# Kernel optimization log

Hardware: AMD Instinct MI355X
Metric: run time of the kernel (lower is better)

The kernel has to match this reference:

```python
import jax, jax.numpy as jnp
import numpy as np

B, N, D, H, C = 32, 512, 256, 256, 2
EPS_NEIGH = 0.3
VSN = 1e-12
SMOOTH_R, DEGREE_R, SPARSITY_R = 0.2, 0.0, 0.1


def setup_inputs() -> dict:
    key = jax.random.key(0)
    ks = jax.random.split(key, 12)
    s = 0.02
    return {
        "context": jax.random.normal(ks[0], (B, N, D), jnp.float32),
        "attention_mask": jnp.ones((B, N, 1), jnp.int32),
        "W_gcn": jax.random.normal(ks[1], (D, H), jnp.float32) * s,
        "b_gcn": jnp.zeros((H,), jnp.float32),
        "W_att1": jax.random.normal(ks[2], (H, H), jnp.float32) * s,
        "b_att1": jnp.zeros((H,), jnp.float32),
        "ln_g": jnp.ones((H,), jnp.float32),
        "ln_b": jnp.zeros((H,), jnp.float32),
        "W_att2": jax.random.normal(ks[3], (H, 1), jnp.float32) * s,
        "b_att2": jnp.zeros((1,), jnp.float32),
        "W_out": jax.random.normal(ks[4], (H, C), jnp.float32) * s,
        "b_out": jnp.zeros((C,), jnp.float32),
    }


def reference(context, attention_mask, W_gcn, b_gcn, W_att1, b_att1,
              ln_g, ln_b, W_att2, b_att2, W_out, b_out):
    # --- GraphLearner (cosine metric + epsilon neighbourhood) ---
    cn = context / jnp.maximum(
        jnp.linalg.norm(context, axis=-1, keepdims=True), VSN)
    att = jnp.einsum('bnd,bmd->bnm', cn, cn)              # [B,N,N]
    mask = jax.lax.stop_gradient((att > EPS_NEIGH).astype(att.dtype))
    adj = att * mask                                      # markoff_value = 0

    # --- GCN diffusion (row-normalized adjacency) ---
    row = adj.sum(-1, keepdims=True)                      # [B,N,1]
    adj_norm = adj / (row + VSN)
    h = jax.nn.relu(
        jnp.einsum('bnm,bmd->bnd', adj_norm, context) @ W_gcn + b_gcn)

    # --- AttentionNetPooling: Linear -> LayerNorm -> GELU -> Linear(1) ---
    a = h @ W_att1 + b_att1
    mu = a.mean(-1, keepdims=True)
    var = a.var(-1, keepdims=True)
    a = (a - mu) / jnp.sqrt(var + 1e-5) * ln_g + ln_b
    w = jax.nn.gelu(a, approximate=False) @ W_att2 + b_att2   # [B,N,1]
    w = jnp.where(attention_mask == 0, -jnp.inf, w)
    w = jax.nn.softmax(w, axis=1)
    pooled = jnp.sum(w * h, axis=1)                       # [B,H]
    logits = pooled @ W_out + b_out                       # [B,C]

    # --- add_batch_graph_loss (L = diag(rowsum) - adj, topk = N) ---
    Lx = row * context - jnp.einsum('bnm,bmd->bnd', adj, context)
    smooth = SMOOTH_R * jnp.mean(
        jnp.sum(context * Lx, axis=(-1, -2)) / (N * N))
    deg = -DEGREE_R * jnp.mean(
        jnp.sum(jnp.log(row[..., 0] + VSN), axis=-1) / N)
    sparsity = SPARSITY_R * jnp.sum(adj ** 2) / (N * N) / B
    graph_loss = smooth + deg + sparsity
    return logits, graph_loss
```

## Files before the change

### kernel.cpp

```cpp
#include <hip/hip_runtime.h>
#include <math.h>

#define NS 512
#define ND 256
#define LIST_CAP 32768u

typedef short short8 __attribute__((ext_vector_type(8)));
typedef float f32x16 __attribute__((ext_vector_type(16)));

__device__ __forceinline__ unsigned short bf16_rne(float x) {
  unsigned u = __float_as_uint(x);
  unsigned r = u + 0x7fffu + ((u >> 16) & 1u);
  return (unsigned short)(r >> 16);
}
__device__ __forceinline__ float bf16_tof(unsigned short h) {
  return __uint_as_float(((unsigned)h) << 16);
}
__device__ __forceinline__ void bsplit(float x, unsigned short& h, unsigned short& l) {
  h = bf16_rne(x);
  l = bf16_rne(x - bf16_tof(h));
}
__device__ __forceinline__ float wave_sum(float v) {
  v += __shfl_xor(v, 1);  v += __shfl_xor(v, 2);  v += __shfl_xor(v, 4);
  v += __shfl_xor(v, 8);  v += __shfl_xor(v, 16); v += __shfl_xor(v, 32);
  return v;
}

__device__ __forceinline__ void gload_lds16(const void* g, void* l) {
  __builtin_amdgcn_global_load_lds(
      (const __attribute__((address_space(1))) unsigned int*)g,
      (__attribute__((address_space(3))) unsigned int*)l, 16, 0, 0);
}

__device__ __forceinline__ void stage4(const unsigned short* __restrict__ hiA,
                                       const unsigned short* __restrict__ loA, int grA,
                                       const unsigned short* __restrict__ hiB,
                                       const unsigned short* __restrict__ loB, int grB,
                                       int k0, char* lds, int wid, int lane)
{
  #pragma unroll
  for (int q = 0; q < 2; ++q) {
    const int c = (q * 4 + wid) * 64 + lane;
    const int row = c >> 3;
    const int soff = ((c & 7) * 16) ^ ((row & 7) << 4);
    const int dest = (q * 4 + wid) * 1024;
    const size_t ga = (size_t)(grA + row) * ND + k0 + (soff >> 1);
    const size_t gb = (size_t)(grB + row) * ND + k0 + (soff >> 1);
    gload_lds16(hiA + ga, lds + dest);
    gload_lds16(loA + ga, lds + 8192 + dest);
    gload_lds16(hiB + gb, lds + 16384 + dest);
    gload_lds16(loB + gb, lds + 24576 + dest);
  }
}

#define SWZB(row, off) (((row) << 7) + (((off) ^ (((row) & 7) << 4))))

#define STEP_MFMA(lds, arow, brow) do { \
  _Pragma("unroll") \
  for (int ks = 0; ks < 4; ++ks) { \
    const int off = ks * 32 + hl * 16; \
    short8 ah = *(const short8*)((lds) + SWZB((arow), off)); \
    short8 al = *(const short8*)((lds) + 8192 + SWZB((arow), off)); \
    short8 bh = *(const short8*)((lds) + 16384 + SWZB((brow), off)); \
    short8 bl = *(const short8*)((lds) + 24576 + SWZB((brow), off)); \
    acc = __builtin_amdgcn_mfma_f32_32x32x16_bf16(ah, bh, acc, 0, 0, 0); \
    acc = __builtin_amdgcn_mfma_f32_32x32x16_bf16(ah, bl, acc, 0, 0, 0); \
    acc = __builtin_amdgcn_mfma_f32_32x32x16_bf16(al, bh, acc, 0, 0, 0); \
  } \
} while (0)

__device__ __forceinline__ float pdot_raw(const float* __restrict__ ctx,
                                          const float* __restrict__ Wg,
                                          int row, int t) {
  const float* cr = ctx + (size_t)row * ND;
  float a = 0.f;
  #pragma unroll 16
  for (int k = 0; k < ND; ++k) a = fmaf(cr[k], Wg[(size_t)k * ND + t], a);
  return a;
}

__global__ __launch_bounds__(256)
void k_prep(const float* __restrict__ ctx, const float* __restrict__ Wg,
            const float* __restrict__ Wa,
            float* __restrict__ nrm, float* __restrict__ nsq,
            unsigned short* __restrict__ cnhi, unsigned short* __restrict__ cnlo,
            unsigned short* __restrict__ wgthi, unsigned short* __restrict__ wgtlo,
            unsigned short* __restrict__ wathi, unsigned short* __restrict__ watlo,
            unsigned* __restrict__ cnt)
{
  if (blockIdx.x >= 4096) {
    int wb = blockIdx.x - 4096;
    int j = wb & 255, selA = wb >> 8;
    int k = threadIdx.x;
    if (wb == 0 && k == 0) *cnt = 0u;
    const float* W = selA ? Wa : Wg;
    unsigned short h, l;
    bsplit(W[k * ND + j], h, l);
    if (selA) { wathi[j * ND + k] = h; watlo[j * ND + k] = l; }
    else      { wgthi[j * ND + k] = h; wgtlo[j * ND + k] = l; }
    return;
  }
  int w = threadIdx.x >> 6, lane = threadIdx.x & 63;
  int g = blockIdx.x * 4 + w;
  float4 v = ((const float4*)ctx)[(size_t)g * 64 + lane];
  float ss = v.x*v.x + v.y*v.y + v.z*v.z + v.w*v.w;
  ss = wave_sum(ss);
  float n = sqrtf(ss);
  float rn = 1.f / fmaxf(n, 1e-12f);
  if (lane == 0) { nrm[g] = n; nsq[g] = ss; }
  ushort4 hi, lo;
  bsplit(v.x * rn, hi.x, lo.x);
  bsplit(v.y * rn, hi.y, lo.y);
  bsplit(v.z * rn, hi.z, lo.z);
  bsplit(v.w * rn, hi.w, lo.w);
  ((ushort4*)cnhi)[(size_t)g * 64 + lane] = hi;
  ((ushort4*)cnlo)[(size_t)g * 64 + lane] = lo;
}

__global__ __launch_bounds__(256, 4)
void k_gram2(const unsigned short* __restrict__ cnhi, const unsigned short* __restrict__ cnlo,
             const float* __restrict__ nrm,
             float* __restrict__ rowp, float* __restrict__ diag,
             float* __restrict__ pA2, float* __restrict__ pA3,
             unsigned* __restrict__ cnt, unsigned* __restrict__ keys,
             float* __restrict__ vals)
{
  __shared__ __align__(16) char lds[32768];
  __shared__ float s_row[2][64];
  __shared__ float s_col[2][64];
  __shared__ float sred[8];
  const int bx0 = blockIdx.x;
  const int bx = (bx0 & 7) * 144 + (bx0 >> 3);
  const int b = bx / 36;
  int rem = bx % 36, ti = 0;
  #pragma unroll
  for (int q = 0; q < 7; ++q) { if (rem >= 8 - ti) { rem -= 8 - ti; ++ti; } }
  const int tj = ti + rem;
  const bool diagT = (ti == tj);
  const int i0 = ti * 64, j0 = tj * 64;
  const int bB = b * NS;
  const int rbA = bB + i0, rbB = bB + j0;

  const int tid = threadIdx.x;
  const int lane = tid & 63, wid = tid >> 6;
  const int l31 = lane & 31, hl = lane >> 5;
  const int wr = wid >> 1, wc = wid & 1;
  const int arow = wr * 32 + l31;
  const int brow = wc * 32 + l31;

  f32x16 acc = {};
  #pragma unroll
  for (int t = 0; t < 4; ++t) {
    stage4(cnhi, cnlo, rbA, cnhi, cnlo, rbB, t * 64, lds, wid, lane);
    __syncthreads();
    STEP_MFMA(lds, arow, brow);
    __syncthreads();
  }

  const float nc = nrm[rbB + wc * 32 + l31];
  const int gcol = wc * 32 + l31;
  float a2 = 0.f, a3 = 0.f, colsum = 0.f;

  #pragma unroll
  for (int r = 0; r < 16; ++r) {
    const int rofs = (r & 3) + 8 * (r >> 2) + 4 * hl;
    const int grow = wr * 32 + rofs;
    const float nr = nrm[rbA + grow];
    float v = acc[r];
    float adj = (v > 0.3f) ? v : 0.f;
    float q2 = adj * adj;
    a3 += q2;
    a2 += q2 * nr * nc;
    colsum += adj;
    if (diagT) {
      if (grow == gcol) {
        diag[bB + i0 + grow] = adj;
      } else if (adj > 0.f) {
        unsigned idx = atomicAdd(cnt, 1u);
        if (idx < LIST_CAP) {
          keys[idx] = (unsigned)((bB + i0 + grow) * NS + (j0 + gcol));
          vals[idx] = adj;
        }
      }
    } else if (adj > 0.f) {
      unsigned idx = atomicAdd(cnt, 2u);
      if (idx < LIST_CAP) {
        keys[idx] = (unsigned)((bB + i0 + grow) * NS + (j0 + gcol));
        vals[idx] = adj;
      }
      if (idx + 1u < LIST_CAP) {
        keys[idx + 1u] = (unsigned)((bB + j0 + gcol) * NS + (i0 + grow));
        vals[idx + 1u] = adj;
      }
    }
    float rs = adj;
    rs += __shfl_xor(rs, 1); rs += __shfl_xor(rs, 2); rs += __shfl_xor(rs, 4);
    rs += __shfl_xor(rs, 8); rs += __shfl_xor(rs, 16);
    if (l31 == 0) s_row[wc][grow] = rs;
  }
  colsum += __shfl_xor(colsum, 32);
  if (!diagT && hl == 0) s_col[wr][gcol] = colsum;
  a2 = wave_sum(a2);
  a3 = wave_sum(a3);
  if (lane == 0) { sred[wid] = a2; sred[4 + wid] = a3; }
  __syncthreads();
  if (tid < 64) {
    rowp[tj * 16384 + rbA + tid] = s_row[0][tid] + s_row[1][tid];
    if (!diagT)
      rowp[ti * 16384 + rbB + tid] = s_col[0][tid] + s_col[1][tid];
  }
  if (tid == 0) {
    float f = diagT ? 1.f : 2.f;
    pA2[bx] = f * (sred[0] + sred[1] + sred[2] + sred[3]);
    pA3[bx] = f * (sred[4] + sred[5] + sred[6] + sred[7]);
  }
}

__global__ __launch_bounds__(256, 4)
void k_pgemm(const unsigned short* __restrict__ cnhi, const unsigned short* __restrict__ cnlo,
             const unsigned short* __restrict__ wgthi, const unsigned short* __restrict__ wgtlo,
             const float* __restrict__ rowp, const float* __restrict__ nrm,
             const float* __restrict__ nsq, const float* __restrict__ diag,
             const float* __restrict__ b_gcn,
             unsigned short* __restrict__ Hhi, unsigned short* __restrict__ Hlo,
             float* __restrict__ pA1)
{
  __shared__ __align__(16) char lds[32768];
  __shared__ float lss[64];
  const int i0 = blockIdx.x * 64;
  const int c0 = blockIdx.y * 64;
  const int tid = threadIdx.x;
  const int lane = tid & 63, wid = tid >> 6;
  const int l31 = lane & 31, hl = lane >> 5;
  const int wr = wid >> 1, wc = wid & 1;
  const int arow = wr * 32 + l31;
  const int brow = wc * 32 + l31;

  if (tid < 64) {
    int g = i0 + tid;
    float r = 0.f;
    #pragma unroll
    for (int s2 = 0; s2 < 8; ++s2) r += rowp[s2 * 16384 + g];
    float rr = 1.f / (r + 1e-12f);
    lss[tid] = nrm[g] * diag[g] * rr;
    float v = r * nsq[g];
    v = wave_sum(v);
    if (tid == 0 && blockIdx.y == 0) pA1[blockIdx.x] = v;
  }

  f32x16 acc = {};
  #pragma unroll
  for (int t = 0; t < 4; ++t) {
    stage4(cnhi, cnlo, i0, wgthi, wgtlo, c0, t * 64, lds, wid, lane);
    __syncthreads();
    STEP_MFMA(lds, arow, brow);
    __syncthreads();
  }

  const int gcol = c0 + wc * 32 + l31;
  const float bv = b_gcn[gcol];
  #pragma unroll
  for (int r = 0; r < 16; ++r) {
    const int rofs = (r & 3) + 8 * (r >> 2) + 4 * hl;
    const int lrow = wr * 32 + rofs;
    const size_t grow = (size_t)(i0 + lrow);
    float v = fmaxf(lss[lrow] * acc[r] + bv, 0.f);
    unsigned short h, l;
    bsplit(v, h, l);
    Hhi[grow * ND + gcol] = h;
    Hlo[grow * ND + gcol] = l;
  }
}

__global__ __launch_bounds__(256)
void k_fix(const float* __restrict__ ctx, const float* __restrict__ Wg,
           const float* __restrict__ rowp, const float* __restrict__ diag,
           const float* __restrict__ b_gcn,
           const unsigned* __restrict__ cnt, const unsigned* __restrict__ keys,
           const float* __restrict__ vals,
           unsigned short* __restrict__ Hhi, unsigned short* __restrict__ Hlo)
{
  unsigned c = *cnt; if (c > LIST_CAP) c = LIST_CAP;
  unsigned e = blockIdx.x;
  if (e >= c) return;
  int bn = (int)(keys[e] >> 9);
  for (unsigned e2 = 0; e2 < e; ++e2)
    if ((int)(keys[e2] >> 9) == bn) return;
  int t = threadIdx.x;
  float r = 0.f;
  #pragma unroll
  for (int s2 = 0; s2 < 8; ++s2) r += rowp[s2 * 16384 + bn];
  float rr = 1.f / (r + 1e-12f);
  float pre = diag[bn] * rr * pdot_raw(ctx, Wg, bn, t) + b_gcn[t];
  for (unsigned e2 = e; e2 < c; ++e2) {
    unsigned k2 = keys[e2];
    if ((int)(k2 >> 9) != bn) continue;
    int bm = (bn & ~511) | (int)(k2 & 511u);
    pre += vals[e2] * rr * pdot_raw(ctx, Wg, bm, t);
  }
  float hv = fmaxf(pre, 0.f);
  unsigned short hh, ll;
  bsplit(hv, hh, ll);
  Hhi[(size_t)bn * ND + t] = hh;
  Hlo[(size_t)bn * ND + t] = ll;
}

__global__ __launch_bounds__(256, 4)
void k_mm1(const unsigned short* __restrict__ Ahi, const unsigned short* __restrict__ Alo,
           const unsigned short* __restrict__ Bthi, const unsigned short* __restrict__ Btlo,
           const float* __restrict__ bias, float* __restrict__ outf)
{
  __shared__ __align__(16) char lds[32768];
  const int i0 = blockIdx.x * 64;
  const int c0 = blockIdx.y * 64;
  const int tid = threadIdx.x;
  const int lane = tid & 63, wid = tid >> 6;
  const int l31 = lane & 31, hl = lane >> 5;
  const int wr = wid >> 1, wc = wid & 1;
  const int arow = wr * 32 + l31;
  const int brow = wc * 32 + l31;

  f32x16 acc = {};
  #pragma unroll
  for (int t = 0; t < 4; ++t) {
    stage4(Ahi, Alo, i0, Bthi, Btlo, c0, t * 64, lds, wid, lane);
    __syncthreads();
    STEP_MFMA(lds, arow, brow);
    __syncthreads();
  }

  const int gcol = c0 + wc * 32 + l31;
  const float bv = bias[gcol];
  #pragma unroll
  for (int r = 0; r < 16; ++r) {
    const int rofs = (r & 3) + 8 * (r >> 2) + 4 * hl;
    const size_t grow = (size_t)(i0 + wr * 32 + rofs);
    outf[grow * ND + gcol] = acc[r] + bv;
  }
}

__global__ __launch_bounds__(256)
void k_ln(const float* __restrict__ a, const float* __restrict__ g,
          const float* __restrict__ bt, const float* __restrict__ W2,
          const float* __restrict__ b2, float* __restrict__ wl)
{
  int w = threadIdx.x >> 6, lane = threadIdx.x & 63;
  int row = blockIdx.x * 4 + w;
  float4 x = ((const float4*)a)[(size_t)row * 64 + lane];
  float s = x.x + x.y + x.z + x.w;
  float ss = fmaf(x.x, x.x, fmaf(x.y, x.y, fmaf(x.z, x.z, x.w * x.w)));
  s = wave_sum(s); ss = wave_sum(ss);
  float mu = s * (1.f / 256.f);
  float var = ss * (1.f / 256.f) - mu * mu;
  float rstd = rsqrtf(fmaxf(var, 0.f) + 1e-5f);
  float4 gg = ((const float4*)g)[lane];
  float4 bb = ((const float4*)bt)[lane];
  float4 wv = ((const float4*)W2)[lane];
  const float inv_sqrt2 = 0.70710678118654752f;
  float d = 0.f;
  float y = (x.x - mu) * rstd * gg.x + bb.x;
  d = fmaf(0.5f * y * (1.f + erff(y * inv_sqrt2)), wv.x, d);
  y = (x.y - mu) * rstd * gg.y + bb.y;
  d = fmaf(0.5f * y * (1.f + erff(y * inv_sqrt2)), wv.y, d);
  y = (x.z - mu) * rstd * gg.z + bb.z;
  d = fmaf(0.5f * y * (1.f + erff(y * inv_sqrt2)), wv.z, d);
  y = (x.w - mu) * rstd * gg.w + bb.w;
  d = fmaf(0.5f * y * (1.f + erff(y * inv_sqrt2)), wv.w, d);
  d = wave_sum(d);
  if (lane == 0) wl[row] = d + b2[0];
}

__global__ __launch_bounds__(512)
void k_poolfin(const float* __restrict__ wl, const int* __restrict__ amask,
               const unsigned short* __restrict__ Hhi, const unsigned short* __restrict__ Hlo,
               const float* __restrict__ W_out, const float* __restrict__ b_out,
               const float* __restrict__ pA1, const float* __restrict__ pA2,
               const float* __restrict__ pA3, float* __restrict__ out)
{
  __shared__ float red[512];
  __shared__ float sw[512];
  __shared__ float pp[512];
  const int t = threadIdx.x;
  if (blockIdx.x < 32) {
    const int b = blockIdx.x;
    float l = (amask[b * NS + t] == 0) ? -INFINITY : wl[b * NS + t];
    red[t] = l;
    __syncthreads();
    for (int s = 256; s; s >>= 1) { if (t < s) red[t] = fmaxf(red[t], red[t + s]); __syncthreads(); }
    float mx = red[0];
    __syncthreads();
    float e = expf(l - mx);
    red[t] = e;
    __syncthreads();
    for (int s = 256; s; s >>= 1) { if (t < s) red[t] += red[t + s]; __syncthreads(); }
    float inv = 1.f / red[0];
    sw[t] = e * inv;
    __syncthreads();
    const int col = t & 255, half = t >> 8;
    const size_t hb = ((size_t)b * NS + (size_t)half * 256) * ND + col;
    float acc = 0.f;
    #pragma unroll 8
    for (int n = 0; n < 256; ++n) {
      float hv = bf16_tof(Hhi[hb + (size_t)n * ND]) + bf16_tof(Hlo[hb + (size_t)n * ND]);
      acc = fmaf(sw[half * 256 + n], hv, acc);
    }
    pp[t] = acc;
    __syncthreads();
    if (t < 256) {
      float pool = pp[t] + pp[256 + t];
      red[t] = pool * W_out[t * 2 + 0];
      red[256 + t] = pool * W_out[t * 2 + 1];
    }
    __syncthreads();
    for (int s = 128; s; s >>= 1) {
      if (t < s) { red[t] += red[t + s]; red[256 + t] += red[256 + t + s]; }
      __syncthreads();
    }
    if (t == 0) {
      out[b * 2 + 0] = red[0] + b_out[0];
      out[b * 2 + 1] = red[256] + b_out[1];
    }
  } else {
    float r1 = (t < 256) ? pA1[t] : 0.f;
    float r2 = pA2[t] + pA2[512 + t] + ((t < 128) ? pA2[1024 + t] : 0.f);
    float r3 = pA3[t] + pA3[512 + t] + ((t < 128) ? pA3[1024 + t] : 0.f);
    red[t] = r1;
    __syncthreads();
    for (int s = 256; s; s >>= 1) { if (t < s) red[t] += red[t + s]; __syncthreads(); }
    r1 = red[0];
    __syncthreads();
    red[t] = r2;
    __syncthreads();
    for (int s = 256; s; s >>= 1) { if (t < s) red[t] += red[t + s]; __syncthreads(); }
    r2 = red[0];
    __syncthreads();
    red[t] = r3;
    __syncthreads();
    for (int s = 256; s; s >>= 1) { if (t < s) red[t] += red[t + s]; __syncthreads(); }
    if (t == 0) {
      float smooth = 0.2f * (r1 - r2) * (1.f / (32.f * 512.f * 512.f));
      float spars  = 0.1f * red[0] * (1.f / (512.f * 512.f)) * (1.f / 32.f);
      out[64] = smooth + spars;
    }
  }
}

extern "C" void kernel_launch(void* const* d_in, const int* in_sizes, int n_in,
                              void* d_out, int out_size, void* d_ws, size_t ws_size,
                              hipStream_t stream)
{
  (void)in_sizes; (void)n_in; (void)out_size; (void)ws_size;
  const float* ctx    = (const float*)d_in[0];
  const int*   amask  = (const int*)d_in[1];
  const float* W_gcn  = (const float*)d_in[2];
  const float* b_gcn  = (const float*)d_in[3];
  const float* W_att1 = (const float*)d_in[4];
  const float* b_att1 = (const float*)d_in[5];
  const float* ln_g   = (const float*)d_in[6];
  const float* ln_b   = (const float*)d_in[7];
  const float* W_att2 = (const float*)d_in[8];
  const float* b_att2 = (const float*)d_in[9];
  const float* W_out  = (const float*)d_in[10];
  const float* b_out  = (const float*)d_in[11];
  float* out = (float*)d_out;

  float* ws = (float*)d_ws;
  unsigned short* cnhi = (unsigned short*)ws;
  unsigned short* cnlo = (unsigned short*)(ws + 2097152);
  unsigned short* Hhi  = (unsigned short*)(ws + 4194304);
  unsigned short* Hlo  = (unsigned short*)(ws + 4194304 + 2097152);
  float* abuf = ws + 8388608;
  float* sp   = ws + 12582912;
  float* nrm  = sp;            sp += 16384;
  float* nsq  = sp;            sp += 16384;
  float* rowp = sp;            sp += 131072;
  float* diag = sp;            sp += 16384;
  float* wl   = sp;            sp += 16384;
  float* pA1  = sp;            sp += 4096;
  float* pA2  = sp;            sp += 1280;
  float* pA3  = sp;            sp += 1280;
  unsigned* cnt  = (unsigned*)sp;  sp += 64;
  unsigned* keys = (unsigned*)sp;  sp += 32768;
  float* vals = sp;            sp += 32768;
  unsigned short* wgthi = (unsigned short*)sp; sp += 32768;
  unsigned short* wgtlo = (unsigned short*)sp; sp += 32768;
  unsigned short* wathi = (unsigned short*)sp; sp += 32768;
  unsigned short* watlo = (unsigned short*)sp; sp += 32768;

  k_prep<<<4608, 256, 0, stream>>>(ctx, W_gcn, W_att1, nrm, nsq, cnhi, cnlo,
                                   wgthi, wgtlo, wathi, watlo, cnt);
  k_gram2<<<1152, 256, 0, stream>>>(cnhi, cnlo, nrm, rowp, diag, pA2, pA3,
                                    cnt, keys, vals);
  k_pgemm<<<dim3(256, 4), 256, 0, stream>>>(cnhi, cnlo, wgthi, wgtlo, rowp,
                                            nrm, nsq, diag, b_gcn, Hhi, Hlo, pA1);
  k_fix<<<256, 256, 0, stream>>>(ctx, W_gcn, rowp, diag, b_gcn,
                                 cnt, keys, vals, Hhi, Hlo);
  k_mm1<<<dim3(256, 4), 256, 0, stream>>>(Hhi, Hlo, wathi, watlo, b_att1, abuf);
  k_ln<<<4096, 256, 0, stream>>>(abuf, ln_g, ln_b, W_att2, b_att2, wl);
  k_poolfin<<<33, 512, 0, stream>>>(wl, amask, Hhi, Hlo, W_out, b_out,
                                    pA1, pA2, pA3, out);
}
```

Before: 97.87 us.

## Split attention pooling across 512 blocks with a separate final reduction kernel

The single 33-block pooling/finalize kernel becomes two kernels. The first uses 512 blocks, each recomputing the per-batch softmax and summing a 32-row slice of H into a partial buffer that reuses the cn workspace. The second reduces the 16 partials per batch, applies W_out, and folds in the graph-loss partial sums. The aim is to fill the GPU during the H read instead of leaving most CUs idle, at the cost of an extra launch and redundant softmax work in every block.

```diff
diff --git a/kernel.cpp b/kernel.cpp
--- a/kernel.cpp
+++ b/kernel.cpp
@@ -370,73 +370,81 @@
   if (lane == 0) wl[row] = d + b2[0];
 }
 
-__global__ __launch_bounds__(512)
-void k_poolfin(const float* __restrict__ wl, const int* __restrict__ amask,
-               const unsigned short* __restrict__ Hhi, const unsigned short* __restrict__ Hlo,
-               const float* __restrict__ W_out, const float* __restrict__ b_out,
-               const float* __restrict__ pA1, const float* __restrict__ pA2,
-               const float* __restrict__ pA3, float* __restrict__ out)
+__global__ __launch_bounds__(256)
+void k_pool2(const float* __restrict__ wl, const int* __restrict__ amask,
+             const unsigned short* __restrict__ hhi, const unsigned short* __restrict__ hlo,
+             float* __restrict__ part)
+{
+  __shared__ float sw[512];
+  __shared__ float red[256];
+  int b = blockIdx.x >> 4, p = blockIdx.x & 15, t = threadIdx.x;
+  float l0 = (amask[b * NS + t]       == 0) ? -INFINITY : wl[b * NS + t];
+  float l1 = (amask[b * NS + 256 + t] == 0) ? -INFINITY : wl[b * NS + 256 + t];
+  red[t] = fmaxf(l0, l1);
+  __syncthreads();
+  for (int s = 128; s; s >>= 1) { if (t < s) red[t] = fmaxf(red[t], red[t + s]); __syncthreads(); }
+  float mx = red[0];
+  __syncthreads();
+  float e0 = expf(l0 - mx), e1 = expf(l1 - mx);
+  red[t] = e0 + e1;
+  __syncthreads();
+  for (int s = 128; s; s >>= 1) { if (t < s) red[t] += red[t + s]; __syncthreads(); }
+  float inv = 1.f / red[0];
+  sw[t] = e0 * inv; sw[256 + t] = e1 * inv;
+  __syncthreads();
+  const size_t base = (size_t)b * NS * ND + (size_t)p * 32 * ND + t;
+  float acc = 0.f;
+  #pragma unroll 8
+  for (int n = 0; n < 32; ++n) {
+    float hv = bf16_tof(hhi[base + (size_t)n * ND]) + bf16_tof(hlo[base + (size_t)n * ND]);
+    acc = fmaf(sw[p * 32 + n], hv, acc);
+  }
+  part[(size_t)blockIdx.x * ND + t] = acc;
+}
+
+__global__ __launch_bounds__(256)
+void k_final(const float* __restrict__ part, const float* __restrict__ W_out,
+             const float* __restrict__ b_out, const float* __restrict__ pA1,
+             const float* __restrict__ pA2, const float* __restrict__ pA3,
+             float* __restrict__ out)
 {
   __shared__ float red[512];
-  __shared__ float sw[512];
-  __shared__ float pp[512];
-  const int t = threadIdx.x;
+  int t = threadIdx.x;
   if (blockIdx.x < 32) {
-    const int b = blockIdx.x;
-    float l = (amask[b * NS + t] == 0) ? -INFINITY : wl[b * NS + t];
-    red[t] = l;
-    __syncthreads();
-    for (int s = 256; s; s >>= 1) { if (t < s) red[t] = fmaxf(red[t], red[t + s]); __syncthreads(); }
-    float mx = red[0];
-    __syncthreads();
-    float e = expf(l - mx);
-    red[t] = e;
-    __syncthreads();
-    for (int s = 256; s; s >>= 1) { if (t < s) red[t] += red[t + s]; __syncthreads(); }
-    float inv = 1.f / red[0];
-    sw[t] = e * inv;
-    __syncthreads();
-    const int col = t & 255, half = t >> 8;
-    const size_t hb = ((size_t)b * NS + (size_t)half * 256) * ND + col;
-    float acc = 0.f;
-    #pragma unroll 8
-    for (int n = 0; n < 256; ++n) {
-      float hv = bf16_tof(Hhi[hb + (size_t)n * ND]) + bf16_tof(Hlo[hb + (size_t)n * ND]);
-      acc = fmaf(sw[half * 256 + n], hv, acc);
-    }
-    pp[t] = acc;
-    __syncthreads();
-    if (t < 256) {
-      float pool = pp[t] + pp[256 + t];
-      red[t] = pool * W_out[t * 2 + 0];
-      red[256 + t] = pool * W_out[t * 2 + 1];
-    }
+    int b = blockIdx.x;
+    float pl = 0.f;
+    #pragma unroll
+    for (int p = 0; p < 16; ++p) pl += part[(size_t)(b * 16 + p) * ND + t];
+    red[t]       = pl * W_out[t * 2 + 0];
+    red[256 + t] = pl * W_out[t * 2 + 1];
     __syncthreads();
     for (int s = 128; s; s >>= 1) {
       if (t < s) { red[t] += red[t + s]; red[256 + t] += red[256 + t + s]; }
       __syncthreads();
     }
     if (t == 0) {
-      out[b * 2 + 0] = red[0] + b_out[0];
+      out[b * 2 + 0] = red[0]   + b_out[0];
       out[b * 2 + 1] = red[256] + b_out[1];
     }
   } else {
-    float r1 = (t < 256) ? pA1[t] : 0.f;
-    float r2 = pA2[t] + pA2[512 + t] + ((t < 128) ? pA2[1024 + t] : 0.f);
-    float r3 = pA3[t] + pA3[512 + t] + ((t < 128) ? pA3[1024 + t] : 0.f);
-    red[t] = r1;
-    __syncthreads();
-    for (int s = 256; s; s >>= 1) { if (t < s) red[t] += red[t + s]; __syncthreads(); }
-    r1 = red[0];
-    __syncthreads();
-    red[t] = r2;
-    __syncthreads();
-    for (int s = 256; s; s >>= 1) { if (t < s) red[t] += red[t + s]; __syncthreads(); }
-    r2 = red[0];
+    float r1 = pA1[t];
+    float r2 = 0.f, r3 = 0.f;
+    #pragma unroll
+    for (int i = 0; i < 5; ++i) {
+      int idx = i * 256 + t;
+      if (idx < 1152) { r2 += pA2[idx]; r3 += pA3[idx]; }
+    }
+    red[t] = r1; red[256 + t] = r2;
+    __syncthreads();
+    for (int s = 128; s; s >>= 1) {
+      if (t < s) { red[t] += red[t + s]; red[256 + t] += red[256 + t + s]; }
+      __syncthreads();
+    }
+    r1 = red[0]; r2 = red[256];
     __syncthreads();
     red[t] = r3;
     __syncthreads();
-    for (int s = 256; s; s >>= 1) { if (t < s) red[t] += red[t + s]; __syncthreads(); }
+    for (int s = 128; s; s >>= 1) { if (t < s) red[t] += red[t + s]; __syncthreads(); }
     if (t == 0) {
       float smooth = 0.2f * (r1 - r2) * (1.f / (32.f * 512.f * 512.f));
       float spars  = 0.1f * red[0] * (1.f / (512.f * 512.f)) * (1.f / 32.f);
@@ -467,6 +475,7 @@
   float* ws = (float*)d_ws;
   unsigned short* cnhi = (unsigned short*)ws;
   unsigned short* cnlo = (unsigned short*)(ws + 2097152);
+  float* part = ws;
   unsigned short* Hhi  = (unsigned short*)(ws + 4194304);
   unsigned short* Hlo  = (unsigned short*)(ws + 4194304 + 2097152);
   float* abuf = ws + 8388608;
@@ -497,6 +506,6 @@
                                  cnt, keys, vals, Hhi, Hlo);
   k_mm1<<<dim3(256, 4), 256, 0, stream>>>(Hhi, Hlo, wathi, watlo, b_att1, abuf);
   k_ln<<<4096, 256, 0, stream>>>(abuf, ln_g, ln_b, W_att2, b_att2, wl);
-  k_poolfin<<<33, 512, 0, stream>>>(wl, amask, Hhi, Hlo, W_out, b_out,
-                                    pA1, pA2, pA3, out);
-}
+  k_pool2<<<512, 256, 0, stream>>>(wl, amask, Hhi, Hlo, part);
+  k_final<<<33, 256, 0, stream>>>(part, W_out, b_out, pA1, pA2, pA3, out);
+}
```

Result: faster. 89.96 us (-8.1%).
